# Optimization experiments

Measured on AMD Instinct MI355X. Metric: run time of the kernel, lower is better.

## Reference

```python
import jax, jax.numpy as jnp
import numpy as np

IN_FEATURES = 1024
HIDDEN_DIM = 1024
B, S = 4, 4096


def setup_inputs() -> dict:
    key = jax.random.key(0)
    ks = jax.random.split(key, 7)
    lim = 1.0 / np.sqrt(IN_FEATURES)
    x = jax.random.normal(ks[0], (B, S, IN_FEATURES), dtype=jnp.float32)
    Wq = jax.random.uniform(ks[1], (IN_FEATURES, HIDDEN_DIM), jnp.float32, -lim, lim)
    bq = jax.random.uniform(ks[2], (HIDDEN_DIM,), jnp.float32, -lim, lim)
    Wk = jax.random.uniform(ks[3], (IN_FEATURES, HIDDEN_DIM), jnp.float32, -lim, lim)
    bk = jax.random.uniform(ks[4], (HIDDEN_DIM,), jnp.float32, -lim, lim)
    Wv = jax.random.uniform(ks[5], (IN_FEATURES, HIDDEN_DIM), jnp.float32, -lim, lim)
    bv = jax.random.uniform(ks[6], (HIDDEN_DIM,), jnp.float32, -lim, lim)
    return {"x": x, "Wq": Wq, "bq": bq, "Wk": Wk, "bk": bk, "Wv": Wv, "bv": bv}


def reference(x, Wq, bq, Wk, bk, Wv, bv):
    # QKV projections: [B, S, H]
    q = jnp.einsum('bsf,fh->bsh', x, Wq) + bq
    k = jnp.einsum('bsf,fh->bsh', x, Wk) + bk
    v = jnp.einsum('bsf,fh->bsh', x, Wv) + bv
    scale = 1.0 / jnp.sqrt(jnp.asarray(q.shape[-1], dtype=q.dtype))
    scores = jnp.einsum('bqh,bkh->bqk', q, k) * scale  # [B, S, S]
    weights = jax.nn.softmax(scores, axis=-1)
    return jnp.einsum('bqk,bkh->bqh', weights, v)
```

## Files before the change

kernel.cpp:

```cpp
#include <hip/hip_runtime.h>

typedef _Float16 half_t;
typedef _Float16 half4_t __attribute__((ext_vector_type(4)));
typedef _Float16 half8_t __attribute__((ext_vector_type(8)));
typedef float float4_t __attribute__((ext_vector_type(4)));

#define S_LEN 4096
#define NB 4
#define H_DIM 1024

#define MFMA16(a, b, c) __builtin_amdgcn_mfma_f32_16x16x32_f16(a, b, c, 0, 0, 0)

#define BAR_LDS()                                      \
  do {                                                 \
    asm volatile("s_waitcnt lgkmcnt(0)" ::: "memory"); \
    __builtin_amdgcn_s_barrier();                      \
  } while (0)

__global__ __launch_bounds__(256) void wt_prep(
    const float* __restrict__ Wq, const float* __restrict__ Wk,
    const float* __restrict__ Wv, half_t* __restrict__ wth,
    half_t* __restrict__ wtl) {
  const int zi = blockIdx.z;
  const float* W = (zi == 0) ? Wq : (zi == 1) ? Wk : Wv;
  half_t* oh = wth + (size_t)zi * H_DIM * H_DIM;
  half_t* ol = wtl + (size_t)zi * H_DIM * H_DIM;
  const int h0 = blockIdx.x * 32, f0 = blockIdx.y * 32;
  __shared__ float Ws[32][33];
  const int t = threadIdx.x;
  const int c = t & 31, r8 = t >> 5;
#pragma unroll
  for (int rr = 0; rr < 4; rr++)
    Ws[r8 * 4 + rr][c] = W[(size_t)(f0 + r8 * 4 + rr) * H_DIM + h0 + c];
  __syncthreads();
#pragma unroll
  for (int rr = 0; rr < 4; rr++) {
    int h = r8 * 4 + rr;
    float v = Ws[c][h];
    half_t hi = (half_t)v;
    half_t lo = (half_t)(v - (float)hi);
    oh[(size_t)(h0 + h) * H_DIM + f0 + c] = hi;
    ol[(size_t)(h0 + h) * H_DIM + f0 + c] = lo;
  }
}

#define QKV_BK 64

__global__ __launch_bounds__(512, 2) void qkv_mfma(
    const float* __restrict__ x, const half_t* __restrict__ wth,
    const half_t* __restrict__ wtl, const float* __restrict__ bq,
    const float* __restrict__ bk, const float* __restrict__ bv,
    half_t* __restrict__ ws) {
  const int bx = blockIdx.x;
  const int zi = bx >> 2;
  const int m0 = (bx & 3) * 256;
  const int n0 = blockIdx.y * 256;
  const half_t* Ah_g = wth + (size_t)zi * H_DIM * H_DIM;
  const half_t* Al_g = wtl + (size_t)zi * H_DIM * H_DIM;
  const float* bias = (zi == 0) ? bq : (zi == 1) ? bk : bv;
  half_t* out = ws + (size_t)zi * ((size_t)NB * S_LEN * H_DIM);
  const int t = threadIdx.x;
  const int w = t >> 6, lane = t & 63, ln = lane & 15, quad = lane >> 4;

  __shared__ half_t Bs[32768];

  float4_t acc[2][16] = {};

  const int ss = t >> 1;
  const int fh = (t & 1) * 32;
  const int snt = ss >> 4, sln = ss & 15;

  for (int k0 = 0; k0 < H_DIM; k0 += QKV_BK) {
    half8_t ah[2][2], al[2][2];
#pragma unroll
    for (int i = 0; i < 2; i++) {
      const size_t arow =
          (size_t)(m0 + w * 32 + i * 16 + ln) * H_DIM + k0 + quad * 8;
#pragma unroll
      for (int k2 = 0; k2 < 2; k2++) {
        ah[i][k2] = *(const half8_t*)(Ah_g + arow + k2 * 32);
        al[i][k2] = *(const half8_t*)(Al_g + arow + k2 * 32);
      }
    }
    BAR_LDS();
    {
      const float* xp = x + (size_t)(n0 + ss) * H_DIM + k0 + fh;
#pragma unroll
      for (int g = 0; g < 4; g++) {
        float4 v0 = *(const float4*)(xp + g * 8);
        float4 v1 = *(const float4*)(xp + g * 8 + 4);
        float vv[8] = {v0.x, v0.y, v0.z, v0.w, v1.x, v1.y, v1.z, v1.w};
        half8_t hhi, hlo;
#pragma unroll
        for (int j = 0; j < 8; j++) {
          half_t h = (half_t)vv[j];
          hhi[j] = h;
          hlo[j] = (half_t)(vv[j] - (float)h);
        }
        int f = fh + g * 8;
        int k2 = f >> 5, qd = (f >> 3) & 3;
        int base = ((k2 * 16 + snt) * 64 + qd * 16 + sln) * 8;
        *(half8_t*)&Bs[base] = hhi;
        *(half8_t*)&Bs[16384 + base] = hlo;
      }
    }
    BAR_LDS();
#pragma unroll
    for (int k2 = 0; k2 < 2; k2++) {
#pragma unroll
      for (int nt = 0; nt < 16; nt++) {
        int base = ((k2 * 16 + nt) * 64 + lane) * 8;
        half8_t bh = *(const half8_t*)&Bs[base];
        half8_t bl = *(const half8_t*)&Bs[16384 + base];
        acc[0][nt] = MFMA16(ah[0][k2], bh, acc[0][nt]);
        acc[1][nt] = MFMA16(ah[1][k2], bh, acc[1][nt]);
        acc[0][nt] = MFMA16(al[0][k2], bh, acc[0][nt]);
        acc[1][nt] = MFMA16(al[1][k2], bh, acc[1][nt]);
        acc[0][nt] = MFMA16(ah[0][k2], bl, acc[0][nt]);
        acc[1][nt] = MFMA16(ah[1][k2], bl, acc[1][nt]);
      }
    }
  }

  const float oscale = (zi == 0) ? 0.03125f : 1.0f;
  float bb[2][4];
#pragma unroll
  for (int i = 0; i < 2; i++)
#pragma unroll
    for (int r = 0; r < 4; r++)
      bb[i][r] = bias[m0 + w * 32 + i * 16 + quad * 4 + r];

  if (zi < 2) {
#pragma unroll
    for (int i = 0; i < 2; i++)
#pragma unroll
      for (int nt = 0; nt < 16; nt++) {
        half4_t h4;
#pragma unroll
        for (int r = 0; r < 4; r++)
          h4[r] = (half_t)((acc[i][nt][r] + bb[i][r]) * oscale);
        size_t s = n0 + nt * 16 + ln;
        *(half4_t*)&out[s * H_DIM + m0 + w * 32 + i * 16 + quad * 4] = h4;
      }
  } else {
#pragma unroll
    for (int i = 0; i < 2; i++)
#pragma unroll
      for (int nt = 0; nt < 16; nt++) {
        int sf = n0 + nt * 16 + ln;
        int b = sf >> 12, si = sf & 4095;
#pragma unroll
        for (int r = 0; r < 4; r++) {
          int h = m0 + w * 32 + i * 16 + quad * 4 + r;
          out[((size_t)b * H_DIM + h) * S_LEN + si] =
              (half_t)(acc[i][nt][r] + bb[i][r]);
        }
      }
  }
}

#define TQ 64
#define TK 128

__global__ __launch_bounds__(512, 2) void flash_attn(
    const half_t* __restrict__ qw, const half_t* __restrict__ kw,
    const half_t* __restrict__ vt, float* __restrict__ out) {
  const int slot = blockIdx.x & 7;
  const int b = slot >> 1;
  const int qb = ((blockIdx.x >> 3) << 1) | (slot & 1);
  const int q0 = qb * TQ;
  const int t = threadIdx.x;
  const int w = t >> 6;
  const int lane = t & 63;
  const int ln = lane & 15;
  const int quad = lane >> 4;

  __shared__ half_t Qs[65536];
  __shared__ half_t Ps[8192];
  __shared__ float wmax[8][64];
  __shared__ float wl[8][64];

  const half_t* qp = qw + ((size_t)b * S_LEN + q0) * H_DIM;
  const half_t* kbp = kw + (size_t)b * S_LEN * H_DIM;
  const half_t* vbt = vt + (size_t)b * H_DIM * S_LEN;

  const half_t* kr = kbp + (size_t)(w * 16 + ln) * H_DIM + quad * 8;
  half8_t kbuf[6];
#pragma unroll
  for (int d = 0; d < 6; d++) kbuf[d] = *(const half8_t*)(kr + d * 32);

#pragma unroll
  for (int i = 0; i < 16; i++) {
    int flat = t * 8 + i * 4096;
    int r = flat >> 10, c = flat & 1023;
    int rs = r >> 4, lq = r & 15, ks = c >> 5, qd = (c >> 3) & 3;
    *(half8_t*)&Qs[((rs * 32 + ks) * 64 + qd * 16 + lq) * 8] =
        *(const half8_t*)&qp[(size_t)r * H_DIM + c];
  }
  BAR_LDS();

  float m_l = -1e30f;
  float l_l = 0.0f;

  float4_t O[4][8] = {};

  for (int kt = 0; kt < S_LEN; kt += TK) {
    float4_t s[4] = {};
    __builtin_amdgcn_s_setprio(1);
#pragma unroll
    for (int ks = 0; ks < 32; ks++) {
      half8_t a0 = *(const half8_t*)&Qs[(ks * 64 + lane) * 8];
      half8_t a1 = *(const half8_t*)&Qs[16384 + (ks * 64 + lane) * 8];
      half8_t a2 = *(const half8_t*)&Qs[32768 + (ks * 64 + lane) * 8];
      half8_t a3 = *(const half8_t*)&Qs[49152 + (ks * 64 + lane) * 8];
      half8_t kc = kbuf[ks % 6];
      if (ks < 26) kbuf[ks % 6] = *(const half8_t*)(kr + (ks + 6) * 32);
      s[0] = MFMA16(a0, kc, s[0]);
      s[1] = MFMA16(a1, kc, s[1]);
      s[2] = MFMA16(a2, kc, s[2]);
      s[3] = MFMA16(a3, kc, s[3]);
    }
    __builtin_amdgcn_s_setprio(0);

    kr += (size_t)TK * H_DIM;
    if (kt + TK < S_LEN) {
#pragma unroll
      for (int d = 0; d < 6; d++) kbuf[d] = *(const half8_t*)(kr + d * 32);
    }

    const half_t* vbase = vbt + (size_t)(w * 128 + ln) * S_LEN + kt + quad * 8;
    half8_t vr[4];
#pragma unroll
    for (int j = 0; j < 4; j++)
      vr[j] = *(const half8_t*)(vbase + (size_t)j * 16 * S_LEN);

    float rm[4][4];
#pragma unroll
    for (int rs = 0; rs < 4; rs++)
#pragma unroll
      for (int r = 0; r < 4; r++) rm[rs][r] = s[rs][r];
#pragma unroll
    for (int off = 1; off < 16; off <<= 1)
#pragma unroll
      for (int rs = 0; rs < 4; rs++)
#pragma unroll
        for (int r = 0; r < 4; r++)
          rm[rs][r] = fmaxf(rm[rs][r], __shfl_xor(rm[rs][r], off));
    if (ln == 0)
#pragma unroll
      for (int rs = 0; rs < 4; rs++)
#pragma unroll
        for (int r = 0; r < 4; r++)
          wmax[w][rs * 16 + quad * 4 + r] = rm[rs][r];
    BAR_LDS();

    float nm_l = m_l;
#pragma unroll
    for (int w2 = 0; w2 < 8; w2++) nm_l = fmaxf(nm_l, wmax[w2][lane]);
    float aS_l = __expf(m_l - nm_l);
    m_l = nm_l;

    const int pbase = (w >> 1) * 512 + (w & 1) * 256 + (ln >> 3) * 128 +
                      quad * 32 + (ln & 7);
    float pl[4][4];
#pragma unroll
    for (int rs = 0; rs < 4; rs++)
#pragma unroll
      for (int r = 0; r < 4; r++) {
        const int q = rs * 16 + quad * 4 + r;
        float nmq = __shfl(m_l, q);
        float aq = __shfl(aS_l, q);
        float p = __expf(s[rs][r] - nmq);
        pl[rs][r] = p;
        Ps[pbase + rs * 2048 + r * 8] = (half_t)p;
#pragma unroll
        for (int j = 0; j < 8; j++) O[rs][j][r] *= aq;
      }
#pragma unroll
    for (int off = 1; off < 16; off <<= 1)
#pragma unroll
      for (int rs = 0; rs < 4; rs++)
#pragma unroll
        for (int r = 0; r < 4; r++) pl[rs][r] += __shfl_xor(pl[rs][r], off);
    if (ln == 0)
#pragma unroll
      for (int rs = 0; rs < 4; rs++)
#pragma unroll
        for (int r = 0; r < 4; r++)
          wl[w][rs * 16 + quad * 4 + r] = pl[rs][r];
    BAR_LDS();

    float s8_l = 0.f;
#pragma unroll
    for (int w2 = 0; w2 < 8; w2++) s8_l += wl[w2][lane];
    l_l = l_l * aS_l + s8_l;

#pragma unroll
    for (int kc = 0; kc < 4; kc++) {
      half8_t pa[4];
#pragma unroll
      for (int rs = 0; rs < 4; rs++)
        pa[rs] = *(const half8_t*)&Ps[((rs * 4 + kc) * 64 + lane) * 8];
      __builtin_amdgcn_s_setprio(1);
#pragma unroll
      for (int j = 0; j < 8; j++) {
        half8_t vc = vr[j & 3];
        const int jn = j + 4;
        if (jn < 8) {
          vr[j & 3] =
              *(const half8_t*)(vbase + (size_t)jn * 16 * S_LEN + kc * 32);
        } else if (kc < 3) {
          vr[j & 3] = *(const half8_t*)(vbase + (size_t)(jn - 8) * 16 * S_LEN +
                                        (kc + 1) * 32);
        }
#pragma unroll
        for (int rs = 0; rs < 4; rs++)
          O[rs][j] = MFMA16(pa[rs], vc, O[rs][j]);
      }
      __builtin_amdgcn_s_setprio(0);
    }
  }

  float il[4][4];
#pragma unroll
  for (int rs = 0; rs < 4; rs++)
#pragma unroll
    for (int r = 0; r < 4; r++)
      il[rs][r] = 1.0f / __shfl(l_l, rs * 16 + quad * 4 + r);
  float* ob = out + ((size_t)b * S_LEN + q0) * H_DIM + w * 128 + ln;
#pragma unroll
  for (int rs = 0; rs < 4; rs++)
#pragma unroll
    for (int j = 0; j < 8; j++)
#pragma unroll
      for (int r = 0; r < 4; r++)
        ob[(size_t)(rs * 16 + quad * 4 + r) * H_DIM + j * 16] =
            O[rs][j][r] * il[rs][r];
}

extern "C" void kernel_launch(void* const* d_in, const int* in_sizes, int n_in,
                              void* d_out, int out_size, void* d_ws,
                              size_t ws_size, hipStream_t stream) {
  const float* x = (const float*)d_in[0];
  const float* Wq = (const float*)d_in[1];
  const float* bq = (const float*)d_in[2];
  const float* Wk = (const float*)d_in[3];
  const float* bk = (const float*)d_in[4];
  const float* Wv = (const float*)d_in[5];
  const float* bv = (const float*)d_in[6];
  half_t* ws = (half_t*)d_ws;
  float* out = (float*)d_out;

  half_t* wth = (half_t*)d_out;
  half_t* wtl = wth + (size_t)3 * H_DIM * H_DIM;

  wt_prep<<<dim3(32, 32, 3), 256, 0, stream>>>(Wq, Wk, Wv, wth, wtl);

  qkv_mfma<<<dim3(12, 64), 512, 0, stream>>>(x, wth, wtl, bq, bk, bv, ws);

  const half_t* qw = ws;
  const half_t* kw = ws + (size_t)NB * S_LEN * H_DIM;
  const half_t* vt = ws + 2 * (size_t)NB * S_LEN * H_DIM;
  flash_attn<<<dim3((S_LEN / TQ) * NB), 512, 0, stream>>>(qw, kw, vt, out);
}
```

Baseline: 998.4 us.

## Double-buffer x tile in LDS and prefetch next k-slice into registers

The QKV projection GEMM now keeps two LDS buffers for the split-fp16 x tile. It loads the next k-slice of x into registers before the MFMA loop and writes it to the alternate buffer afterward, so there is one barrier per iteration instead of two. The aim is to overlap global x loads with MFMA work. In exchange, LDS use doubles to 128 KB per block, which may cut the 2-blocks-per-CU occupancy, and the prefetched x values add register pressure.

Measured after the change: 957.4 us. -4.1%, faster.

```diff
diff --git a/kernel.cpp b/kernel.cpp
--- a/kernel.cpp
+++ b/kernel.cpp
@@ -62,7 +62,7 @@
   const int t = threadIdx.x;
   const int w = t >> 6, lane = t & 63, ln = lane & 15, quad = lane >> 4;
 
-  __shared__ half_t Bs[32768];
+  __shared__ half_t Bs[2][32768];
 
   float4_t acc[2][16] = {};
 
@@ -70,7 +70,38 @@
   const int fh = (t & 1) * 32;
   const int snt = ss >> 4, sln = ss & 15;
 
-  for (int k0 = 0; k0 < H_DIM; k0 += QKV_BK) {
+  const float* xrow = x + (size_t)(n0 + ss) * H_DIM + fh;
+
+  float4 xr[8];
+#pragma unroll
+  for (int g = 0; g < 4; g++) {
+    xr[2 * g] = *(const float4*)(xrow + g * 8);
+    xr[2 * g + 1] = *(const float4*)(xrow + g * 8 + 4);
+  }
+#pragma unroll
+  for (int g = 0; g < 4; g++) {
+    float vv[8] = {xr[2 * g].x,     xr[2 * g].y,     xr[2 * g].z,
+                   xr[2 * g].w,     xr[2 * g + 1].x, xr[2 * g + 1].y,
+                   xr[2 * g + 1].z, xr[2 * g + 1].w};
+    half8_t hhi, hlo;
+#pragma unroll
+    for (int j = 0; j < 8; j++) {
+      half_t h = (half_t)vv[j];
+      hhi[j] = h;
+      hlo[j] = (half_t)(vv[j] - (float)h);
+    }
+    int f = fh + g * 8;
+    int k2 = f >> 5, qd = (f >> 3) & 3;
+    int base = ((k2 * 16 + snt) * 64 + qd * 16 + sln) * 8;
+    *(half8_t*)&Bs[0][base] = hhi;
+    *(half8_t*)&Bs[0][16384 + base] = hlo;
+  }
+
+  for (int it = 0; it < 16; it++) {
+    const int k0 = it * QKV_BK;
+    const int cur = it & 1;
+    const bool more = (it < 15);
+
     half8_t ah[2][2], al[2][2];
 #pragma unroll
     for (int i = 0; i < 2; i++) {
@@ -82,14 +113,39 @@
         al[i][k2] = *(const half8_t*)(Al_g + arow + k2 * 32);
       }
     }
+    if (more) {
+      const float* xp = xrow + (k0 + QKV_BK);
+#pragma unroll
+      for (int g = 0; g < 4; g++) {
+        xr[2 * g] = *(const float4*)(xp + g * 8);
+        xr[2 * g + 1] = *(const float4*)(xp + g * 8 + 4);
+      }
+    }
+
     BAR_LDS();
-    {
-      const float* xp = x + (size_t)(n0 + ss) * H_DIM + k0 + fh;
+
+#pragma unroll
+    for (int k2 = 0; k2 < 2; k2++) {
+#pragma unroll
+      for (int nt = 0; nt < 16; nt++) {
+        int base = ((k2 * 16 + nt) * 64 + lane) * 8;
+        half8_t bh = *(const half8_t*)&Bs[cur][base];
+        half8_t bl = *(const half8_t*)&Bs[cur][16384 + base];
+        acc[0][nt] = MFMA16(ah[0][k2], bh, acc[0][nt]);
+        acc[1][nt] = MFMA16(ah[1][k2], bh, acc[1][nt]);
+        acc[0][nt] = MFMA16(al[0][k2], bh, acc[0][nt]);
+        acc[1][nt] = MFMA16(al[1][k2], bh, acc[1][nt]);
+        acc[0][nt] = MFMA16(ah[0][k2], bl, acc[0][nt]);
+        acc[1][nt] = MFMA16(ah[1][k2], bl, acc[1][nt]);
+      }
+    }
+
+    if (more) {
 #pragma unroll
       for (int g = 0; g < 4; g++) {
-        float4 v0 = *(const float4*)(xp + g * 8);
-        float4 v1 = *(const float4*)(xp + g * 8 + 4);
-        float vv[8] = {v0.x, v0.y, v0.z, v0.w, v1.x, v1.y, v1.z, v1.w};
+        float vv[8] = {xr[2 * g].x,     xr[2 * g].y,     xr[2 * g].z,
+                       xr[2 * g].w,     xr[2 * g + 1].x, xr[2 * g + 1].y,
+                       xr[2 * g + 1].z, xr[2 * g + 1].w};
         half8_t hhi, hlo;
 #pragma unroll
         for (int j = 0; j < 8; j++) {
@@ -100,24 +156,8 @@
         int f = fh + g * 8;
         int k2 = f >> 5, qd = (f >> 3) & 3;
         int base = ((k2 * 16 + snt) * 64 + qd * 16 + sln) * 8;
-        *(half8_t*)&Bs[base] = hhi;
-        *(half8_t*)&Bs[16384 + base] = hlo;
-      }
-    }
-    BAR_LDS();
-#pragma unroll
-    for (int k2 = 0; k2 < 2; k2++) {
-#pragma unroll
-      for (int nt = 0; nt < 16; nt++) {
-        int base = ((k2 * 16 + nt) * 64 + lane) * 8;
-        half8_t bh = *(const half8_t*)&Bs[base];
-        half8_t bl = *(const half8_t*)&Bs[16384 + base];
-        acc[0][nt] = MFMA16(ah[0][k2], bh, acc[0][nt]);
-        acc[1][nt] = MFMA16(ah[1][k2], bh, acc[1][nt]);
-        acc[0][nt] = MFMA16(al[0][k2], bh, acc[0][nt]);
-        acc[1][nt] = MFMA16(al[1][k2], bh, acc[1][nt]);
-        acc[0][nt] = MFMA16(ah[0][k2], bl, acc[0][nt]);
-        acc[1][nt] = MFMA16(ah[1][k2], bl, acc[1][nt]);
+        *(half8_t*)&Bs[cur ^ 1][base] = hhi;
+        *(half8_t*)&Bs[cur ^ 1][16384 + base] = hlo;
       }
     }
   }
```
